# Kernel tuning notes

Hardware: AMD Instinct MI355X
Metric: run time of the kernel (lower is better)

## Reference

```python
import itertools
import jax, jax.numpy as jnp
import numpy as np

# static block configuration
B, C, H, W, DIM, HEADS = 2, 4, 60, 120, 512, 8
WS = (2, 6, 12)          # window size (Wc, Wh, Ww)
SS = (1, 3, 6)           # shift size
N = WS[0] * WS[1] * WS[2]            # 144 tokens per window
C1, H1, W1 = C // WS[0], H // WS[1], W // WS[2]
NW = C1 * H1 * W1                    # windows per sample
DH = DIM // HEADS
EPS = 1e-6


def _attn_bias():
    """Static shifted-window attention bias (nW, N, N): 0 within group, -inf across.
    Mirrors compute_3d_shifted_window_mask (warped=True, longitude wrap merge)."""
    img = np.zeros((C, H, W), np.int32)
    c_sl = ((0, C - WS[0]), (C - WS[0], C - SS[0]), (C - SS[0], C))
    h_sl = ((0, H - WS[1]), (H - WS[1], H - SS[1]), (H - SS[1], H))
    w_sl = ((0, W - WS[2]), (W - WS[2], W - SS[2]), (W - SS[2], W))
    cnt = 0
    for (cs, ce), (hs, he), (ws_, we) in itertools.product(c_sl, h_sl, w_sl):
        img[cs:ce, hs:he, ws_:we] = cnt
        cnt += 1
    # warped (periodic longitude) group merges
    for i in range(3):
        for a, b in ((1, 2), (4, 5), (7, 8)):
            img[img == a + 9 * i] = b + 9 * i
    m = img.reshape(C1, WS[0], H1, WS[1], W1, WS[2])
    m = m.transpose(0, 2, 4, 1, 3, 5).reshape(NW, N)
    diff = m[:, None, :] - m[:, :, None]
    return jnp.asarray(np.where(diff != 0, -np.inf, 0.0).astype(np.float32))


_BIAS = _attn_bias()[None, :, None, :, :]  # (1, nW, 1, N, N)


def _ln(x, s, b):
    mu = x.mean(-1, keepdims=True)
    var = x.var(-1, keepdims=True)
    return (x - mu) / jnp.sqrt(var + EPS) * s + b


def setup_inputs() -> dict:
    key = jax.random.key(0)
    ks = jax.random.split(key, 6)
    s = 0.02
    return {
        "x": jax.random.normal(ks[0], (B, C * H * W, DIM), jnp.float32),
        "qkv_w": jax.random.normal(ks[1], (DIM, 3 * DIM), jnp.float32) * s,
        "qkv_b": jnp.zeros((3 * DIM,), jnp.float32),
        "proj_w": jax.random.normal(ks[2], (DIM, DIM), jnp.float32) * s,
        "proj_b": jnp.zeros((DIM,), jnp.float32),
        "norm1_scale": jnp.ones((DIM,), jnp.float32),
        "norm1_bias": jnp.zeros((DIM,), jnp.float32),
        "norm2_scale": jnp.ones((DIM,), jnp.float32),
        "norm2_bias": jnp.zeros((DIM,), jnp.float32),
        "mlp_w1": jax.random.normal(ks[3], (DIM, 4 * DIM), jnp.float32) * s,
        "mlp_b1": jnp.zeros((4 * DIM,), jnp.float32),
        "mlp_w2": jax.random.normal(ks[4], (4 * DIM, DIM), jnp.float32) * s,
        "mlp_b2": jnp.zeros((DIM,), jnp.float32),
    }


def reference(x, qkv_w, qkv_b, proj_w, proj_b, norm1_scale, norm1_bias,
              norm2_scale, norm2_bias, mlp_w1, mlp_b1, mlp_w2, mlp_b2):
    shortcut = x                                   # (B, L, D)
    h = _ln(x, norm1_scale, norm1_bias).reshape(B, C, H, W, DIM)
    # cyclic shift
    h = jnp.roll(h, (-SS[0], -SS[1], -SS[2]), axis=(1, 2, 3))
    # window partition: (B,C,H,W,D) -> (B*nW, N, D)
    h = h.reshape(B, C1, WS[0], H1, WS[1], W1, WS[2], DIM)
    h = h.transpose(0, 1, 3, 5, 2, 4, 6, 7).reshape(B * NW, N, DIM)
    # windowed multi-head self-attention
    qkv = h @ qkv_w + qkv_b                        # (B*nW, N, 3*D)
    qkv = qkv.reshape(B, NW, N, 3, HEADS, DH)
    q = qkv[..., 0, :, :].transpose(0, 1, 3, 2, 4)  # (B, nW, H, N, Dh)
    k = qkv[..., 1, :, :].transpose(0, 1, 3, 2, 4)
    v = qkv[..., 2, :, :].transpose(0, 1, 3, 2, 4)
    scale = 1.0 / float(np.sqrt(DH))
    attn = jnp.einsum("bwhnd,bwhmd->bwhnm", q, k) * scale + _BIAS
    attn = jax.nn.softmax(attn, axis=-1)
    o = jnp.einsum("bwhnm,bwhmd->bwhnd", attn, v)
    o = o.transpose(0, 1, 3, 2, 4).reshape(B * NW, N, DIM)
    o = o @ proj_w + proj_b
    # window reverse: (B*nW, N, D) -> (B,C,H,W,D)
    o = o.reshape(B, C1, H1, W1, WS[0], WS[1], WS[2], DIM)
    o = o.transpose(0, 1, 4, 2, 5, 3, 6, 7).reshape(B, C, H, W, DIM)
    # reverse cyclic shift
    o = jnp.roll(o, SS, axis=(1, 2, 3))
    x = shortcut + o.reshape(B, C * H * W, DIM)    # drop_path is identity
    # MLP block
    h2 = _ln(x, norm2_scale, norm2_bias)
    h2 = jax.nn.gelu(h2 @ mlp_w1 + mlp_b1) @ mlp_w2 + mlp_b2
    return x + h2
```

## Files before the change

kernel.cpp:

```cpp
#include <hip/hip_runtime.h>

typedef __attribute__((ext_vector_type(8))) short bf16x8;
typedef __attribute__((ext_vector_type(4))) float f32x4;
typedef __attribute__((ext_vector_type(8))) unsigned short u16x8;

__device__ inline unsigned short f2bf(float f) {
  unsigned int u = __float_as_uint(f);
  u += 0x7fffu + ((u >> 16) & 1u);
  return (unsigned short)(u >> 16);
}

__device__ inline void gload_lds16(const void* g, void* l) {
  __builtin_amdgcn_global_load_lds(
      (const __attribute__((address_space(1))) void*)g,
      (__attribute__((address_space(3))) void*)l, 16, 0, 0);
}

__global__ void wtrans(const float* __restrict__ W, unsigned short* __restrict__ Wt,
                       int K, int N) {
  int idx = blockIdx.x * 256 + threadIdx.x;
  if (idx >= K * N) return;
  int k = idx / N, n = idx - k * N;
  Wt[(size_t)n * K + k] = f2bf(W[idx]);
}

template <int MODE>
__global__ void ln_k(const float* __restrict__ x, const float* __restrict__ sc,
                     const float* __restrict__ bi, unsigned short* __restrict__ o) {
  int t = blockIdx.x * 4 + (threadIdx.x >> 6);
  int l = threadIdx.x & 63;
  size_t src;
  if (MODE == 0) {
    int b = t / 28800, r = t - b * 28800;
    int win = r / 144, tok = r - win * 144;
    int c1 = win / 100, rem = win - c1 * 100;
    int h1 = rem / 10, w1 = rem - h1 * 10;
    int tc = tok / 72, tr = tok - tc * 72;
    int th = tr / 12, tw = tr - th * 12;
    int cs = c1 * 2 + tc, hs = h1 * 6 + th, wsp = w1 * 12 + tw;
    int co = (cs + 1) & 3;
    int ho = hs + 3; if (ho >= 60) ho -= 60;
    int wo = wsp + 6; if (wo >= 120) wo -= 120;
    src = ((size_t)b * 28800 + (co * 60 + ho) * 120 + wo) * 512;
  } else {
    src = (size_t)t * 512;
  }
  const float4* xr = (const float4*)(x + src);
  float4 v0 = xr[l * 2], v1 = xr[l * 2 + 1];
  float s = v0.x + v0.y + v0.z + v0.w + v1.x + v1.y + v1.z + v1.w;
  float s2 = v0.x * v0.x + v0.y * v0.y + v0.z * v0.z + v0.w * v0.w +
             v1.x * v1.x + v1.y * v1.y + v1.z * v1.z + v1.w * v1.w;
  #pragma unroll
  for (int o2 = 32; o2; o2 >>= 1) {
    s += __shfl_xor(s, o2);
    s2 += __shfl_xor(s2, o2);
  }
  float mean = s * (1.0f / 512.0f);
  float var = s2 * (1.0f / 512.0f) - mean * mean;
  float inv = rsqrtf(var + 1e-6f);
  const float4* scp = (const float4*)sc;
  const float4* bip = (const float4*)bi;
  float4 sa = scp[l * 2], sb = scp[l * 2 + 1];
  float4 ba = bip[l * 2], bb = bip[l * 2 + 1];
  u16x8 ov;
  ov[0] = f2bf((v0.x - mean) * inv * sa.x + ba.x);
  ov[1] = f2bf((v0.y - mean) * inv * sa.y + ba.y);
  ov[2] = f2bf((v0.z - mean) * inv * sa.z + ba.z);
  ov[3] = f2bf((v0.w - mean) * inv * sa.w + ba.w);
  ov[4] = f2bf((v1.x - mean) * inv * sb.x + bb.x);
  ov[5] = f2bf((v1.y - mean) * inv * sb.y + bb.y);
  ov[6] = f2bf((v1.z - mean) * inv * sb.z + bb.z);
  ov[7] = f2bf((v1.w - mean) * inv * sb.w + bb.w);
  *(u16x8*)&o[(size_t)t * 512 + l * 8] = ov;
}

template <int EPI>
__launch_bounds__(256)
__global__ void gemm128(const unsigned short* __restrict__ A,
                        const unsigned short* __restrict__ Bt,
                        const float* __restrict__ bias, void* __restrict__ outp,
                        const float* __restrict__ res, int M, int N, int K) {
  __shared__ __attribute__((aligned(16))) unsigned short As[128 * 32];
  __shared__ __attribute__((aligned(16))) unsigned short Bs[128 * 32];
  int tid = threadIdx.x;
  int w = tid >> 6, l = tid & 63;
  int ntile = N >> 7;
  int bm = blockIdx.x / ntile, bn = blockIdx.x - bm * ntile;
  const unsigned short* Ab = A + (size_t)bm * 128 * K;
  const unsigned short* Bb = Bt + (size_t)bn * 128 * K;
  int lr = l >> 2, lc = (l & 3) << 3;
  int lane15 = l & 15, lk = (l >> 4) << 3;
  int wr = (w >> 1) << 6, wc = (w & 1) << 6;
  f32x4 acc[4][4] = {};
  for (int k0 = 0; k0 < K; k0 += 32) {
    #pragma unroll
    for (int i = 0; i < 2; ++i) {
      int row = i * 64 + w * 16 + lr;
      gload_lds16(Ab + (size_t)row * K + k0 + lc, &As[(i * 64 + w * 16) * 32]);
      gload_lds16(Bb + (size_t)row * K + k0 + lc, &Bs[(i * 64 + w * 16) * 32]);
    }
    __syncthreads();
    bf16x8 af[4], bf[4];
    #pragma unroll
    for (int mt = 0; mt < 4; ++mt)
      af[mt] = *(const bf16x8*)&As[(wr + mt * 16 + lane15) * 32 + lk];
    #pragma unroll
    for (int nt = 0; nt < 4; ++nt)
      bf[nt] = *(const bf16x8*)&Bs[(wc + nt * 16 + lane15) * 32 + lk];
    #pragma unroll
    for (int mt = 0; mt < 4; ++mt)
      #pragma unroll
      for (int nt = 0; nt < 4; ++nt)
        acc[mt][nt] =
            __builtin_amdgcn_mfma_f32_16x16x32_bf16(af[mt], bf[nt], acc[mt][nt], 0, 0, 0);
    __syncthreads();
  }
  float* outf = (float*)outp;
  unsigned short* outh = (unsigned short*)outp;
  #pragma unroll
  for (int mt = 0; mt < 4; ++mt) {
    #pragma unroll
    for (int j = 0; j < 4; ++j) {
      int grow = bm * 128 + wr + mt * 16 + ((l >> 4) << 2) + j;
      int win = 0, tok = 0;
      size_t rowbase = 0;
      if constexpr (EPI == 0) {
        win = grow / 144;
        tok = grow - win * 144;
      } else if constexpr (EPI == 1) {
        win = grow / 144;
        tok = grow - win * 144;
        int b = win / 200, wl = win - b * 200;
        int c1 = wl / 100, rem = wl - c1 * 100;
        int h1 = rem / 10, w1 = rem - h1 * 10;
        int tc = tok / 72, tr = tok - tc * 72;
        int th = tr / 12, tw = tr - th * 12;
        int cs = c1 * 2 + tc, hs = h1 * 6 + th, wsp = w1 * 12 + tw;
        int co = (cs + 1) & 3;
        int ho = hs + 3; if (ho >= 60) ho -= 60;
        int wo = wsp + 6; if (wo >= 120) wo -= 120;
        rowbase = ((size_t)b * 28800 + (co * 60 + ho) * 120 + wo) * 512;
      }
      #pragma unroll
      for (int nt = 0; nt < 4; ++nt) {
        int gcol = bn * 128 + wc + nt * 16 + lane15;
        float val = acc[mt][nt][j] + bias[gcol];
        if constexpr (EPI == 0) {
          int which = gcol >> 9, hd = (gcol >> 6) & 7, dh = gcol & 63;
          outh[(((size_t)(win * 3 + which) * 8 + hd) * 144 + tok) * 64 + dh] = f2bf(val);
        } else if constexpr (EPI == 1) {
          size_t oi = rowbase + gcol;
          outf[oi] = res[oi] + val;
        } else if constexpr (EPI == 2) {
          float u = 0.7978845608f * (val + 0.044715f * val * val * val);
          float g = 0.5f * val * (1.0f + tanhf(u));
          outh[(size_t)grow * N + gcol] = f2bf(g);
        } else {
          size_t oi = (size_t)grow * N + gcol;
          outf[oi] += val;
        }
      }
    }
  }
}

__launch_bounds__(576)
__global__ void attn_k(const unsigned short* __restrict__ qkv,
                       unsigned short* __restrict__ owin) {
  __shared__ __attribute__((aligned(16))) unsigned short Ks[144 * 72];
  __shared__ __attribute__((aligned(16))) unsigned short Vt[64 * 168];
  __shared__ __attribute__((aligned(16))) unsigned short Ps[144 * 168];
  __shared__ unsigned char gid[144];
  int bid = blockIdx.x;
  int win = bid >> 3, head = bid & 7;
  const unsigned short* qb = qkv + ((size_t)(win * 3 + 0) * 8 + head) * (144 * 64);
  const unsigned short* kb = qkv + ((size_t)(win * 3 + 1) * 8 + head) * (144 * 64);
  const unsigned short* vb = qkv + ((size_t)(win * 3 + 2) * 8 + head) * (144 * 64);
  int tid = threadIdx.x;
  {
    int row = tid >> 2, c0 = (tid & 3) << 4;
    u16x8 ka = *(const u16x8*)(kb + row * 64 + c0);
    u16x8 kc = *(const u16x8*)(kb + row * 64 + c0 + 8);
    *(u16x8*)&Ks[row * 72 + c0] = ka;
    *(u16x8*)&Ks[row * 72 + c0 + 8] = kc;
    u16x8 va = *(const u16x8*)(vb + row * 64 + c0);
    u16x8 vc = *(const u16x8*)(vb + row * 64 + c0 + 8);
    #pragma unroll
    for (int j = 0; j < 8; ++j) Vt[(c0 + j) * 168 + row] = va[j];
    #pragma unroll
    for (int j = 0; j < 8; ++j) Vt[(c0 + 8 + j) * 168 + row] = vc[j];
  }
  for (int i = tid; i < 64 * 24; i += 576) {
    int d = i / 24, m = i - d * 24;
    Vt[d * 168 + 144 + m] = 0;
  }
  for (int i = tid; i < 144 * 24; i += 576) {
    int r = i / 24, c = i - r * 24;
    Ps[r * 168 + 144 + c] = 0;
  }
  if (tid < 144) {
    int wl = win % 200;
    int c1 = wl / 100, rem = wl - c1 * 100;
    int h1 = rem / 10, w1 = rem - h1 * 10;
    int tc = tid / 72, tr = tid - tc * 72;
    int th = tr / 12, tw = tr - th * 12;
    int cs = c1 * 2 + tc, hs = h1 * 6 + th, wsp = w1 * 12 + tw;
    int rc = cs < 2 ? 0 : (cs < 3 ? 1 : 2);
    int rh = hs < 54 ? 0 : (hs < 57 ? 1 : 2);
    int rw = wsp < 108 ? 0 : (wsp < 114 ? 1 : 2);
    if (rw == 1) rw = 2;
    gid[tid] = (unsigned char)(rc * 9 + rh * 3 + rw);
  }
  __syncthreads();
  int wv = tid >> 6, l = tid & 63;
  int lane15 = l & 15, lk = (l >> 4) << 3;
  bf16x8 aq0 = *(const bf16x8*)(qb + (wv * 16 + lane15) * 64 + lk);
  bf16x8 aq1 = *(const bf16x8*)(qb + (wv * 16 + lane15) * 64 + 32 + lk);
  f32x4 sf[9];
  #pragma unroll
  for (int ct = 0; ct < 9; ++ct) {
    f32x4 z = {};
    bf16x8 b0 = *(const bf16x8*)&Ks[(ct * 16 + lane15) * 72 + lk];
    bf16x8 b1 = *(const bf16x8*)&Ks[(ct * 16 + lane15) * 72 + 32 + lk];
    z = __builtin_amdgcn_mfma_f32_16x16x32_bf16(aq0, b0, z, 0, 0, 0);
    z = __builtin_amdgcn_mfma_f32_16x16x32_bf16(aq1, b1, z, 0, 0, 0);
    sf[ct] = z;
  }
  int gi[4];
  #pragma unroll
  for (int j = 0; j < 4; ++j) gi[j] = gid[wv * 16 + ((l >> 4) << 2) + j];
  float mx[4] = {-1e30f, -1e30f, -1e30f, -1e30f};
  #pragma unroll
  for (int ct = 0; ct < 9; ++ct) {
    int gj = gid[ct * 16 + lane15];
    #pragma unroll
    for (int j = 0; j < 4; ++j) {
      float s = sf[ct][j] * 0.125f;
      if (gj != gi[j]) s = -1e30f;
      sf[ct][j] = s;
      mx[j] = fmaxf(mx[j], s);
    }
  }
  #pragma unroll
  for (int o2 = 8; o2; o2 >>= 1)
    #pragma unroll
    for (int j = 0; j < 4; ++j) mx[j] = fmaxf(mx[j], __shfl_xor(mx[j], o2));
  float sm[4] = {0.f, 0.f, 0.f, 0.f};
  #pragma unroll
  for (int ct = 0; ct < 9; ++ct)
    #pragma unroll
    for (int j = 0; j < 4; ++j) {
      float e = __expf(sf[ct][j] - mx[j]);
      sf[ct][j] = e;
      sm[j] += e;
    }
  #pragma unroll
  for (int o2 = 8; o2; o2 >>= 1)
    #pragma unroll
    for (int j = 0; j < 4; ++j) sm[j] += __shfl_xor(sm[j], o2);
  float rs[4];
  #pragma unroll
  for (int j = 0; j < 4; ++j) rs[j] = 1.0f / sm[j];
  #pragma unroll
  for (int ct = 0; ct < 9; ++ct)
    #pragma unroll
    for (int j = 0; j < 4; ++j)
      Ps[(wv * 16 + ((l >> 4) << 2) + j) * 168 + ct * 16 + lane15] =
          f2bf(sf[ct][j] * rs[j]);
  __syncthreads();
  f32x4 of[4] = {};
  #pragma unroll
  for (int ks = 0; ks < 5; ++ks) {
    bf16x8 ap = *(const bf16x8*)&Ps[(wv * 16 + lane15) * 168 + ks * 32 + lk];
    #pragma unroll
    for (int nt = 0; nt < 4; ++nt) {
      bf16x8 bv = *(const bf16x8*)&Vt[(nt * 16 + lane15) * 168 + ks * 32 + lk];
      of[nt] = __builtin_amdgcn_mfma_f32_16x16x32_bf16(ap, bv, of[nt], 0, 0, 0);
    }
  }
  unsigned short* ob = owin + (size_t)win * 144 * 512 + head * 64;
  #pragma unroll
  for (int nt = 0; nt < 4; ++nt)
    #pragma unroll
    for (int j = 0; j < 4; ++j) {
      int row = wv * 16 + ((l >> 4) << 2) + j;
      ob[(size_t)row * 512 + nt * 16 + lane15] = f2bf(of[nt][j]);
    }
}

extern "C" void kernel_launch(void* const* d_in, const int* in_sizes, int n_in,
                              void* d_out, int out_size, void* d_ws, size_t ws_size,
                              hipStream_t stream) {
  const float* x = (const float*)d_in[0];
  const float* qkv_w = (const float*)d_in[1];
  const float* qkv_b = (const float*)d_in[2];
  const float* proj_w = (const float*)d_in[3];
  const float* proj_b = (const float*)d_in[4];
  const float* n1s = (const float*)d_in[5];
  const float* n1b = (const float*)d_in[6];
  const float* n2s = (const float*)d_in[7];
  const float* n2b = (const float*)d_in[8];
  const float* w1 = (const float*)d_in[9];
  const float* b1 = (const float*)d_in[10];
  const float* w2 = (const float*)d_in[11];
  const float* b2 = (const float*)d_in[12];
  float* out = (float*)d_out;
  char* ws = (char*)d_ws;

  unsigned short* WqT = (unsigned short*)(ws);
  unsigned short* WpT = (unsigned short*)(ws + 1572864);
  unsigned short* W1T = (unsigned short*)(ws + 2097152);
  unsigned short* W2T = (unsigned short*)(ws + 4194304);
  unsigned short* hwin = (unsigned short*)(ws + 6291456);
  unsigned short* qkvb = (unsigned short*)(ws + 65273856);
  unsigned short* owin = (unsigned short*)(ws + 242221056);
  unsigned short* mid = qkvb;

  wtrans<<<(512 * 1536 + 255) / 256, 256, 0, stream>>>(qkv_w, WqT, 512, 1536);
  wtrans<<<(512 * 512 + 255) / 256, 256, 0, stream>>>(proj_w, WpT, 512, 512);
  wtrans<<<(512 * 2048 + 255) / 256, 256, 0, stream>>>(w1, W1T, 512, 2048);
  wtrans<<<(2048 * 512 + 255) / 256, 256, 0, stream>>>(w2, W2T, 2048, 512);
  ln_k<0><<<14400, 256, 0, stream>>>(x, n1s, n1b, hwin);
  gemm128<0><<<450 * 12, 256, 0, stream>>>(hwin, WqT, qkv_b, qkvb, nullptr, 57600, 1536, 512);
  attn_k<<<3200, 576, 0, stream>>>(qkvb, owin);
  gemm128<1><<<450 * 4, 256, 0, stream>>>(owin, WpT, proj_b, out, x, 57600, 512, 512);
  ln_k<1><<<14400, 256, 0, stream>>>(out, n2s, n2b, hwin);
  gemm128<2><<<450 * 16, 256, 0, stream>>>(hwin, W1T, b1, mid, nullptr, 57600, 2048, 512);
  gemm128<3><<<450 * 4, 256, 0, stream>>>(mid, W2T, b2, out, nullptr, 57600, 512, 2048);
}
```

Measured before the change: 951.1 us.

## Double-buffer GEMM LDS tiles with swizzle and XCD-aware block remap

Replaces the GEMM kernel with a double-buffered version that prefetches the next K tile into LDS while the MFMAs run on the current one, leaving one barrier per iteration instead of two. It XOR-swizzles the LDS column layout to cut bank conflicts, and remaps block IDs so consecutive tiles land on the same XCD for better L2 reuse. The GELU tanh is rewritten as an equivalent sigmoid form using a fast exp. LDS use doubles, which could reduce occupancy.

```diff
diff --git a/kernel.cpp b/kernel.cpp
--- a/kernel.cpp
+++ b/kernel.cpp
@@ -76,52 +76,76 @@
 
 template <int EPI>
 __launch_bounds__(256)
-__global__ void gemm128(const unsigned short* __restrict__ A,
-                        const unsigned short* __restrict__ Bt,
-                        const float* __restrict__ bias, void* __restrict__ outp,
-                        const float* __restrict__ res, int M, int N, int K) {
-  __shared__ __attribute__((aligned(16))) unsigned short As[128 * 32];
-  __shared__ __attribute__((aligned(16))) unsigned short Bs[128 * 32];
-  int tid = threadIdx.x;
-  int w = tid >> 6, l = tid & 63;
-  int ntile = N >> 7;
-  int bm = blockIdx.x / ntile, bn = blockIdx.x - bm * ntile;
-  const unsigned short* Ab = A + (size_t)bm * 128 * K;
-  const unsigned short* Bb = Bt + (size_t)bn * 128 * K;
-  int lr = l >> 2, lc = (l & 3) << 3;
-  int lane15 = l & 15, lk = (l >> 4) << 3;
-  int wr = (w >> 1) << 6, wc = (w & 1) << 6;
+__global__ void gemm97(const unsigned short* __restrict__ A,
+                       const unsigned short* __restrict__ Bt,
+                       const float* __restrict__ bias, void* __restrict__ outp,
+                       const float* __restrict__ res, int M, int N, int K) {
+  __shared__ __attribute__((aligned(16))) unsigned short sA[2][4096];
+  __shared__ __attribute__((aligned(16))) unsigned short sB[2][4096];
+  const int tid = threadIdx.x;
+  const int w = tid >> 6, l = tid & 63;
+  const int wm = w >> 1, wn = w & 1;
+  const int lane15 = l & 15, lk = (l >> 4) << 3;
+  const int ntile = N >> 7;
+  const int nwg = gridDim.x;
+  const int q = nwg >> 3, r = nwg & 7;
+  const int xcd = blockIdx.x & 7, idx8 = blockIdx.x >> 3;
+  const int wgid = (xcd < r ? xcd * (q + 1) : r * (q + 1) + (xcd - r) * q) + idx8;
+  const int bm = wgid / ntile, bn = wgid - bm * ntile;
+  const int KT = K >> 5;
+
+  const int srow = w * 16 + (l >> 2);
+  const int scol = ((l & 3) << 3) ^ (((srow >> 1) & 3) << 3);
+  const int offA0 = (srow * K + scol) * 2;
+  const int offA1 = offA0 + 64 * K * 2;
+
+  const char* gA = (const char*)(A + (size_t)bm * 128 * K);
+  const char* gB = (const char*)(Bt + (size_t)bn * 128 * K);
+
+  const int sw = ((lane15 >> 1) & 3) << 3;
+  const int rcol = (lk ^ sw);
+
   f32x4 acc[4][4] = {};
-  for (int k0 = 0; k0 < K; k0 += 32) {
-    #pragma unroll
-    for (int i = 0; i < 2; ++i) {
-      int row = i * 64 + w * 16 + lr;
-      gload_lds16(Ab + (size_t)row * K + k0 + lc, &As[(i * 64 + w * 16) * 32]);
-      gload_lds16(Bb + (size_t)row * K + k0 + lc, &Bs[(i * 64 + w * 16) * 32]);
-    }
+
+  auto STAGE = [&](int buf, int t) {
+    const char* ga = gA + (size_t)t * 64;
+    const char* gb = gB + (size_t)t * 64;
+    gload_lds16(ga + offA0, &sA[buf][w * 512]);
+    gload_lds16(ga + offA1, &sA[buf][2048 + w * 512]);
+    gload_lds16(gb + offA0, &sB[buf][w * 512]);
+    gload_lds16(gb + offA1, &sB[buf][2048 + w * 512]);
+  };
+
+  STAGE(0, 0);
+  __syncthreads();
+
+  int buf = 0;
+  for (int t = 0; t < KT; ++t) {
+    if (t + 1 < KT) STAGE(buf ^ 1, t + 1);
+    bf16x8 af[4], bf[4];
+    #pragma unroll
+    for (int mf = 0; mf < 4; ++mf)
+      af[mf] = *(const bf16x8*)&sA[buf][(wm * 64 + mf * 16 + lane15) * 32 + rcol];
+    #pragma unroll
+    for (int nf = 0; nf < 4; ++nf)
+      bf[nf] = *(const bf16x8*)&sB[buf][(wn * 64 + nf * 16 + lane15) * 32 + rcol];
+    #pragma unroll
+    for (int mf = 0; mf < 4; ++mf)
+      #pragma unroll
+      for (int nf = 0; nf < 4; ++nf)
+        acc[mf][nf] = __builtin_amdgcn_mfma_f32_16x16x32_bf16(
+            af[mf], bf[nf], acc[mf][nf], 0, 0, 0);
     __syncthreads();
-    bf16x8 af[4], bf[4];
-    #pragma unroll
-    for (int mt = 0; mt < 4; ++mt)
-      af[mt] = *(const bf16x8*)&As[(wr + mt * 16 + lane15) * 32 + lk];
-    #pragma unroll
-    for (int nt = 0; nt < 4; ++nt)
-      bf[nt] = *(const bf16x8*)&Bs[(wc + nt * 16 + lane15) * 32 + lk];
-    #pragma unroll
-    for (int mt = 0; mt < 4; ++mt)
-      #pragma unroll
-      for (int nt = 0; nt < 4; ++nt)
-        acc[mt][nt] =
-            __builtin_amdgcn_mfma_f32_16x16x32_bf16(af[mt], bf[nt], acc[mt][nt], 0, 0, 0);
-    __syncthreads();
-  }
+    buf ^= 1;
+  }
+
   float* outf = (float*)outp;
   unsigned short* outh = (unsigned short*)outp;
   #pragma unroll
-  for (int mt = 0; mt < 4; ++mt) {
+  for (int mf = 0; mf < 4; ++mf) {
     #pragma unroll
     for (int j = 0; j < 4; ++j) {
-      int grow = bm * 128 + wr + mt * 16 + ((l >> 4) << 2) + j;
+      int grow = bm * 128 + wm * 64 + mf * 16 + ((l >> 4) << 2) + j;
       int win = 0, tok = 0;
       size_t rowbase = 0;
       if constexpr (EPI == 0) {
@@ -142,9 +166,9 @@
         rowbase = ((size_t)b * 28800 + (co * 60 + ho) * 120 + wo) * 512;
       }
       #pragma unroll
-      for (int nt = 0; nt < 4; ++nt) {
-        int gcol = bn * 128 + wc + nt * 16 + lane15;
-        float val = acc[mt][nt][j] + bias[gcol];
+      for (int nf = 0; nf < 4; ++nf) {
+        int gcol = bn * 128 + wn * 64 + nf * 16 + lane15;
+        float val = acc[mf][nf][j] + bias[gcol];
         if constexpr (EPI == 0) {
           int which = gcol >> 9, hd = (gcol >> 6) & 7, dh = gcol & 63;
           outh[(((size_t)(win * 3 + which) * 8 + hd) * 144 + tok) * 64 + dh] = f2bf(val);
@@ -153,7 +177,7 @@
           outf[oi] = res[oi] + val;
         } else if constexpr (EPI == 2) {
           float u = 0.7978845608f * (val + 0.044715f * val * val * val);
-          float g = 0.5f * val * (1.0f + tanhf(u));
+          float g = val / (1.0f + __expf(-2.0f * u));
           outh[(size_t)grow * N + gcol] = f2bf(g);
         } else {
           size_t oi = (size_t)grow * N + gcol;
@@ -321,10 +345,10 @@
   wtrans<<<(512 * 2048 + 255) / 256, 256, 0, stream>>>(w1, W1T, 512, 2048);
   wtrans<<<(2048 * 512 + 255) / 256, 256, 0, stream>>>(w2, W2T, 2048, 512);
   ln_k<0><<<14400, 256, 0, stream>>>(x, n1s, n1b, hwin);
-  gemm128<0><<<450 * 12, 256, 0, stream>>>(hwin, WqT, qkv_b, qkvb, nullptr, 57600, 1536, 512);
+  gemm97<0><<<450 * 12, 256, 0, stream>>>(hwin, WqT, qkv_b, qkvb, nullptr, 57600, 1536, 512);
   attn_k<<<3200, 576, 0, stream>>>(qkvb, owin);
-  gemm128<1><<<450 * 4, 256, 0, stream>>>(owin, WpT, proj_b, out, x, 57600, 512, 512);
+  gemm97<1><<<450 * 4, 256, 0, stream>>>(owin, WpT, proj_b, out, x, 57600, 512, 512);
   ln_k<1><<<14400, 256, 0, stream>>>(out, n2s, n2b, hwin);
-  gemm128<2><<<450 * 16, 256, 0, stream>>>(hwin, W1T, b1, mid, nullptr, 57600, 2048, 512);
-  gemm128<3><<<450 * 4, 256, 0, stream>>>(mid, W2T, b2, out, nullptr, 57600, 512, 2048);
-}
+  gemm97<2><<<450 * 16, 256, 0, stream>>>(hwin, W1T, b1, mid, nullptr, 57600, 2048, 512);
+  gemm97<3><<<450 * 4, 256, 0, stream>>>(mid, W2T, b2, out, nullptr, 57600, 512, 2048);
+}
```

Result: faster. 907.7 us (-4.6%).
